# Kernel tuning notes

Hardware: AMD Instinct MI355X
Metric: run time of the kernel (lower is better)

## Reference

```python
import jax, jax.numpy as jnp
import numpy as np

B, L, D = 2, 2048, 2048
NH, NKV = 16, 8
HD = D // NH            # 128
GQ = NH // NKV          # queries per kv head
THETA = 10000.0
SCALE = HD ** -0.5


def rope_tables(seq_len, dim, theta):
    inv_freq = 1.0 / theta ** (jnp.arange(0, dim, 2, dtype=jnp.float32) / dim)
    t = jnp.arange(seq_len, dtype=jnp.float32)
    freqs = jnp.outer(t, inv_freq)              # [L, dim/2]
    emb = jnp.concatenate([freqs, freqs], -1)   # [L, dim]
    return jnp.cos(emb), jnp.sin(emb)


def rotate_half(x):
    x1, x2 = jnp.split(x, 2, axis=-1)
    return jnp.concatenate([-x2, x1], -1)


def setup_inputs() -> dict:
    key = jax.random.key(0)
    ks = jax.random.split(key, 5)
    s = 0.02
    return {
        "x": jax.random.normal(ks[0], (B, L, D), jnp.float32),
        "Wq": jax.random.normal(ks[1], (NH * HD, D), jnp.float32) * s,
        "Wk": jax.random.normal(ks[2], (NKV * HD, D), jnp.float32) * s,
        "Wv": jax.random.normal(ks[3], (NKV * HD, D), jnp.float32) * s,
        "Wo": jax.random.normal(ks[4], (D, D), jnp.float32) * s,
    }


def reference(x, Wq, Wk, Wv, Wo):
    b, l, d = x.shape
    q = (x @ Wq.T).reshape(b, l, NH, HD).transpose(0, 2, 1, 3)    # [B,NH,L,HD]
    k = (x @ Wk.T).reshape(b, l, NKV, HD).transpose(0, 2, 1, 3)   # [B,NKV,L,HD]
    v = (x @ Wv.T).reshape(b, l, NKV, HD).transpose(0, 2, 1, 3)

    cos, sin = rope_tables(l, HD, THETA)                           # [L,HD]
    q = q * cos + rotate_half(q) * sin
    k = k * cos + rotate_half(k) * sin

    # GQA without materializing expanded K/V: group queries per kv head
    qg = q.reshape(b, NKV, GQ, l, HD)
    scores = jnp.einsum('bgrld,bgmd->bgrlm', qg, k) * SCALE        # [B,NKV,GQ,L,L]
    causal = jnp.triu(jnp.ones((l, l), bool), k=1)
    scores = jnp.where(causal, -jnp.inf, scores)
    attn = jax.nn.softmax(scores.astype(jnp.float32), axis=-1).astype(q.dtype)
    out = jnp.einsum('bgrlm,bgmd->bgrld', attn, v)                 # [B,NKV,GQ,L,HD]
    out = out.reshape(b, NH, l, HD).transpose(0, 2, 1, 3).reshape(b, l, d)
    return out @ Wo.T
```

## Files before the change

kernel.cpp:

```cpp
#include <hip/hip_runtime.h>
#include <cmath>

using u16 = unsigned short;
typedef u16    u16x4  __attribute__((ext_vector_type(4)));
typedef u16    u16x8  __attribute__((ext_vector_type(8)));
typedef __bf16 bf16x8 __attribute__((ext_vector_type(8)));
typedef float  f32x4  __attribute__((ext_vector_type(4)));

constexpr int Bc  = 2;
constexpr int Lc  = 2048;
constexpr int Dc  = 2048;
constexpr int NHc = 16;
constexpr int NKVc= 8;
constexpr int HDc = 128;

__device__ __forceinline__ u16 f2b(float f) {
  union { float f; unsigned u; } v; v.f = f;
  unsigned r = v.u + 0x7FFFu + ((v.u >> 16) & 1u);
  return (u16)(r >> 16);
}
__device__ __forceinline__ u16 f2b_fast(float f) {
  union { float f; unsigned u; } v; v.f = f;
  return (u16)((v.u + 0x8000u) >> 16);
}
__device__ __forceinline__ float b2f(u16 s) {
  union { unsigned u; float f; } v; v.u = ((unsigned)s) << 16;
  return v.f;
}
__device__ __forceinline__ bf16x8 ld_frag(const u16* p) {
  u16x8 u = *(const u16x8*)p;
  return __builtin_bit_cast(bf16x8, u);
}
__device__ __forceinline__ void gld_lds16(u16* ldst, const u16* gsrc) {
  __builtin_amdgcn_global_load_lds(
      (const __attribute__((address_space(1))) void*)gsrc,
      (__attribute__((address_space(3))) void*)ldst, 16, 0, 0);
}

__global__ void cvt_f32_bf16(const float* __restrict__ src, u16* __restrict__ dst, int n) {
  int i = (blockIdx.x * blockDim.x + threadIdx.x) * 4;
  if (i >= n) return;
  float4 v = *(const float4*)&src[i];
  u16x4 o = { f2b(v.x), f2b(v.y), f2b(v.z), f2b(v.w) };
  *(u16x4*)&dst[i] = o;
}

__global__ void cvt_w3(const float* __restrict__ Wq, const float* __restrict__ Wk,
                       const float* __restrict__ Wv, u16* __restrict__ dst) {
  const int n1 = Dc * Dc;
  const int n2 = n1 + (NKVc*HDc) * Dc;
  const int n3 = n2 + (NKVc*HDc) * Dc;
  int i = (blockIdx.x * blockDim.x + threadIdx.x) * 4;
  if (i >= n3) return;
  const float* src; int off;
  if (i < n1)      { src = Wq; off = i; }
  else if (i < n2) { src = Wk; off = i - n1; }
  else             { src = Wv; off = i - n2; }
  float4 v = *(const float4*)&src[off];
  u16x4 o = { f2b(v.x), f2b(v.y), f2b(v.z), f2b(v.w) };
  *(u16x4*)&dst[i] = o;
}

__device__ __forceinline__ void stage_tile32(u16* lds, const u16* __restrict__ A,
    const u16* __restrict__ W, int slot, int kt, int m0, int n0, int wave, int lane)
{
  const int srow = lane >> 2;
  const int scg  = lane & 3;
  const int skey = (lane >> 3) & 3;
  const int sb   = slot * 16384;
#pragma unroll
  for (int i = 0; i < 2; ++i) {
    int c = wave + i * 8;
    int row = c * 16 + srow;
    gld_lds16(&lds[sb + c * 512],
              &A[(size_t)(m0 + row) * Dc + kt * 32 + (scg ^ skey) * 8]);
    gld_lds16(&lds[sb + 8192 + c * 512],
              &W[(size_t)(n0 + row) * Dc + kt * 32 + (scg ^ skey) * 8]);
  }
}

__device__ __forceinline__ void compute_tile32(const u16* lds, int slot,
    int wm, int wn, int quad, int l16, f32x4 acc[8][4])
{
  const u16* sA = lds + slot * 16384;
  const u16* sB = sA + 8192;
  const int pcg = (quad ^ ((l16 >> 1) & 3)) * 8;
  bf16x8 af[8], bfr[4];
#pragma unroll
  for (int mi = 0; mi < 8; ++mi)
    af[mi] = ld_frag(&sA[(wm * 128 + mi * 16 + l16) * 32 + pcg]);
#pragma unroll
  for (int ni = 0; ni < 4; ++ni)
    bfr[ni] = ld_frag(&sB[(wn * 64 + ni * 16 + l16) * 32 + pcg]);
  __builtin_amdgcn_s_setprio(1);
#pragma unroll
  for (int mi = 0; mi < 8; ++mi)
#pragma unroll
    for (int ni = 0; ni < 4; ++ni)
      acc[mi][ni] = __builtin_amdgcn_mfma_f32_16x16x32_bf16(af[mi], bfr[ni], acc[mi][ni], 0, 0, 0);
  __builtin_amdgcn_s_setprio(0);
}

__global__ __launch_bounds__(512, 2) void gemm256_qkv(
    const u16* __restrict__ A, const u16* __restrict__ W,
    u16* __restrict__ Qp, u16* __restrict__ Kp, u16* __restrict__ Vtp)
{
  __shared__ u16 lds[65536];
  const int tid  = threadIdx.x;
  const int wave = tid >> 6, lane = tid & 63;
  const int quad = lane >> 4, l16 = lane & 15;
  const int bid = blockIdx.x;
  const int swz = (bid & 7) * 32 + (bid >> 3);
  const int tx = swz & 15, ty = swz >> 4;
  const int m0 = ty * 256, n0 = tx * 256;
  const int wm = wave >> 2, wn = wave & 3;

  f32x4 acc[8][4];
#pragma unroll
  for (int i = 0; i < 8; ++i)
#pragma unroll
    for (int j = 0; j < 4; ++j) acc[i][j] = {0.f, 0.f, 0.f, 0.f};

  stage_tile32(lds, A, W, 0, 0, m0, n0, wave, lane);
  stage_tile32(lds, A, W, 1, 1, m0, n0, wave, lane);
  stage_tile32(lds, A, W, 2, 2, m0, n0, wave, lane);

  for (int kt = 0; kt < 61; ++kt) {
    __asm__ volatile("s_waitcnt vmcnt(8)\n\ts_barrier" ::: "memory");
    stage_tile32(lds, A, W, (kt + 3) & 3, kt + 3, m0, n0, wave, lane);
    compute_tile32(lds, kt & 3, wm, wn, quad, l16, acc);
  }
  __asm__ volatile("s_waitcnt vmcnt(8)\n\ts_barrier" ::: "memory");
  compute_tile32(lds, 1, wm, wn, quad, l16, acc);
  __asm__ volatile("s_waitcnt vmcnt(4)\n\ts_barrier" ::: "memory");
  compute_tile32(lds, 2, wm, wn, quad, l16, acc);
  __asm__ volatile("s_waitcnt vmcnt(0)\n\ts_barrier" ::: "memory");
  compute_tile32(lds, 3, wm, wn, quad, l16, acc);

  if (n0 < 3072) {
    u16* Cb; int ldc, nc0;
    if (n0 < 2048) { Cb = Qp; ldc = 2048; nc0 = n0; }
    else           { Cb = Kp; ldc = 1024; nc0 = n0 - 2048; }
#pragma unroll
    for (int mi = 0; mi < 8; ++mi)
#pragma unroll
      for (int ni = 0; ni < 4; ++ni)
#pragma unroll
        for (int r = 0; r < 4; ++r) {
          int m = m0 + wm * 128 + mi * 16 + quad * 4 + r;
          int n = nc0 + wn * 64 + ni * 16 + l16;
          Cb[(size_t)m * ldc + n] = f2b(acc[mi][ni][r]);
        }
  } else {
    __syncthreads();
#pragma unroll
    for (int mi = 0; mi < 8; ++mi)
#pragma unroll
      for (int ni = 0; ni < 4; ++ni)
#pragma unroll
        for (int r = 0; r < 4; ++r) {
          int l = wm * 128 + mi * 16 + quad * 4 + r;
          int d = wn * 64 + ni * 16 + l16;
          lds[l * 256 + (((d >> 3) ^ (l & 31)) << 3) + (d & 7)] = f2b(acc[mi][ni][r]);
        }
    __syncthreads();
    const int b    = m0 >> 11;
    const int hkv0 = (n0 - 3072) >> 7;
#pragma unroll
    for (int it = 0; it < 16; ++it) {
      int sl = tid + it * 512;
      int dl = sl >> 5;
      int lc = (sl & 31) * 8;
      u16x8 v;
#pragma unroll
      for (int e = 0; e < 8; ++e) {
        int l = lc + e;
        v[e] = lds[l * 256 + (((dl >> 3) ^ (l & 31)) << 3) + (dl & 7)];
      }
      const int hkv = hkv0 + (dl >> 7);
      const int d   = dl & 127;
      *(u16x8*)&Vtp[(((size_t)b * NKVc + hkv) * HDc + d) * (size_t)Lc + (m0 & (Lc - 1)) + lc] = v;
    }
  }
}

__global__ __launch_bounds__(256) void gemm_out(
    const u16* __restrict__ A, const u16* __restrict__ W,
    float* __restrict__ Cf, int M, int N, int K)
{
  __shared__ u16 lds[16384];
  u16* lA = lds;
  u16* lB = lds + 8192;
  const int tid  = threadIdx.x;
  const int wave = tid >> 6, lane = tid & 63;
  const int quad = lane >> 4, l16 = lane & 15;
  const int t7   = l16 & 7;
  const int m0 = blockIdx.y * 128, n0 = blockIdx.x * 128;
  const int mw = (wave >> 1) * 64, nw = (wave & 1) * 64;
  const int r8 = lane >> 3;
  const int cgl = (lane & 7) ^ r8;

  f32x4 acc[4][4];
#pragma unroll
  for (int i = 0; i < 4; ++i)
#pragma unroll
    for (int j = 0; j < 4; ++j) acc[i][j] = {0.f, 0.f, 0.f, 0.f};

  for (int kt = 0; kt < K; kt += 64) {
#pragma unroll
    for (int cc = 0; cc < 4; ++cc) {
      int c = wave + cc * 4;
      gld_lds16(&lA[c * 512], &A[(size_t)(m0 + 8 * c + r8) * K + kt + cgl * 8]);
      gld_lds16(&lB[c * 512], &W[(size_t)(n0 + 8 * c + r8) * K + kt + cgl * 8]);
    }
    __syncthreads();
#pragma unroll
    for (int s = 0; s < 2; ++s) {
      bf16x8 af[4], bf[4];
#pragma unroll
      for (int i = 0; i < 4; ++i)
        af[i] = ld_frag(&lA[(mw + i*16 + l16) * 64 + ((quad + 4*s) ^ t7) * 8]);
#pragma unroll
      for (int j = 0; j < 4; ++j)
        bf[j] = ld_frag(&lB[(nw + j*16 + l16) * 64 + ((quad + 4*s) ^ t7) * 8]);
#pragma unroll
      for (int i = 0; i < 4; ++i)
#pragma unroll
        for (int j = 0; j < 4; ++j)
          acc[i][j] = __builtin_amdgcn_mfma_f32_16x16x32_bf16(af[i], bf[j], acc[i][j], 0, 0, 0);
    }
    __syncthreads();
  }

#pragma unroll
  for (int i = 0; i < 4; ++i)
#pragma unroll
    for (int j = 0; j < 4; ++j)
#pragma unroll
      for (int r = 0; r < 4; ++r) {
        int m = m0 + mw + i*16 + quad*4 + r;
        int n = n0 + nw + j*16 + l16;
        Cf[(size_t)m * N + n] = acc[i][j][r];
      }
}

__global__ void rope2_kernel(u16* __restrict__ Qp, u16* __restrict__ Kp, float qs)
{
  const int nQ = Bc * Lc * NHc * 64;
  const int nT = nQ + Bc * Lc * NKVc * 64;
  int t = blockIdx.x * blockDim.x + threadIdx.x;
  if (t >= nT) return;
  u16* T; int nheads; float osc; int idx;
  if (t < nQ) { T = Qp; nheads = NHc;  osc = qs;  idx = t; }
  else        { T = Kp; nheads = NKVc; osc = 1.f; idx = t - nQ; }
  int d   = idx & 63;
  int h   = (idx >> 6) % nheads;
  int row = idx / (nheads * 64);
  int l   = row & (Lc - 1);
  float freq = exp2f((float)d * (-13.287712379549449f / 64.f));
  float ang  = (float)l * freq;
  float s, c;
  sincosf(ang, &s, &c);
  size_t base = (size_t)row * (nheads * 128) + h * 128;
  float x1 = b2f(T[base + d]);
  float x2 = b2f(T[base + d + 64]);
  T[base + d]      = f2b((x1 * c - x2 * s) * osc);
  T[base + d + 64] = f2b((x2 * c + x1 * s) * osc);
}

__global__ __launch_bounds__(512) void flash_kernel(
    const u16* __restrict__ Q, const u16* __restrict__ K, const u16* __restrict__ Vt,
    u16* __restrict__ O)
{
  __shared__ u16 smem[41984];
  const int tid  = threadIdx.x;
  const int wave = tid >> 6, lane = tid & 63;
  const int quad = lane >> 4, l16 = lane & 15;
  const int hw = wave >> 2, wr = wave & 3;
  const int bhkv = blockIdx.x;
  const int b = bhkv >> 3, hkv = bhkv & 7;
  const int h = hkv * 2 + hw;

  const size_t kbase = ((size_t)b * Lc) * (NKVc * HDc) + (size_t)hkv * HDc;
  const size_t vbase = (((size_t)b * NKVc + hkv) * HDc) * (size_t)Lc;

  const int kr8 = lane >> 4;
  const int kcl = lane & 15;
  const int vr16 = lane >> 3;
  const int vkl  = lane & 7;

  u16* sP_w = smem + 32768 + wave * 1152;

  for (int pass = 0; pass < 2; ++pass) {
    const int qt = (pass == 0) ? (31 - (int)blockIdx.y) : (int)blockIdx.y;
    const int q0 = qt * 64;

    __syncthreads();
#pragma unroll
    for (int i = 0; i < 4; ++i) {
      int g = tid + i * 512;
      int row = g >> 4, cg = g & 15;
      int qh = hkv * 2 + (row >> 6);
      int rr = row & 63;
      *(u16x8*)&smem[row * 128 + (cg ^ (row & 15)) * 8] =
          *(const u16x8*)&Q[((size_t)(b * Lc + q0 + rr)) * Dc + (size_t)qh * HDc + cg * 8];
    }
    __syncthreads();
    bf16x8 qf[4];
#pragma unroll
    for (int ks = 0; ks < 4; ++ks)
      qf[ks] = ld_frag(&smem[(hw*64 + wr*16 + l16) * 128 + ((ks*4 + quad) ^ l16) * 8]);
    __syncthreads();

#pragma unroll
    for (int i = 0; i < 2; ++i) {
      int c = wave + i * 8;
      int row = c * 4 + kr8;
      gld_lds16(smem + c * 512,
                &K[kbase + (size_t)row * (NKVc*HDc) + (size_t)(kcl ^ (row & 15)) * 8]);
    }
#pragma unroll
    for (int i = 0; i < 2; ++i) {
      int c = wave + i * 8;
      int d = c * 8 + vr16;
      gld_lds16(smem + 16384 + c * 512,
                &Vt[vbase + (size_t)d * Lc + (size_t)(vkl ^ (d & 7)) * 8]);
    }

    f32x4 acc_o[8];
#pragma unroll
    for (int i = 0; i < 8; ++i) acc_o[i] = {0.f, 0.f, 0.f, 0.f};
    float ps[4] = {0.f, 0.f, 0.f, 0.f};

    for (int kt = 0; kt <= qt; ++kt) {
      const int kOff  = (kt & 1) ? 8192 : 0;
      const int kOffN = (kt & 1) ? 0 : 8192;
      const int vOff  = (kt & 1) ? 24576 : 16384;
      const int vOffN = (kt & 1) ? 16384 : 24576;

      __asm__ volatile("s_waitcnt vmcnt(2)\n\ts_barrier" ::: "memory");

      if (kt < qt) {
#pragma unroll
        for (int i = 0; i < 2; ++i) {
          int c = wave + i * 8;
          int row = (kt + 1) * 64 + c * 4 + kr8;
          gld_lds16(smem + kOffN + c * 512,
                    &K[kbase + (size_t)row * (NKVc*HDc) + (size_t)(kcl ^ (row & 15)) * 8]);
        }
      }

      const u16* sKc = smem + kOff;
      f32x4 accs[4];
#pragma unroll
      for (int n = 0; n < 4; ++n) accs[n] = {0.f, 0.f, 0.f, 0.f};
#pragma unroll
      for (int ks = 0; ks < 4; ++ks)
#pragma unroll
        for (int n = 0; n < 4; ++n) {
          bf16x8 kf = ld_frag(&sKc[(n*16 + l16) * 128 + ((ks*4 + quad) ^ l16) * 8]);
          accs[n] = __builtin_amdgcn_mfma_f32_16x16x32_bf16(qf[ks], kf, accs[n], 0, 0, 0);
        }

      const int qrow = q0 + wr*16 + quad*4;
      if (kt == qt) {
#pragma unroll
        for (int n = 0; n < 4; ++n) {
          int kg = kt*64 + n*16 + l16;
#pragma unroll
          for (int r = 0; r < 4; ++r)
            if (kg > qrow + r) accs[n][r] = -INFINITY;
        }
      }
#pragma unroll
      for (int n = 0; n < 4; ++n)
#pragma unroll
        for (int r = 0; r < 4; ++r) {
          float p = exp2f(accs[n][r]);
          accs[n][r] = p;
          ps[r] += p;
        }

#pragma unroll
      for (int n = 0; n < 4; ++n)
#pragma unroll
        for (int r = 0; r < 4; ++r)
          sP_w[(quad*4 + r) * 72 + n*16 + l16] = f2b_fast(accs[n][r]);

      if (kt < qt)
        __asm__ volatile("s_waitcnt vmcnt(2) lgkmcnt(0)\n\ts_barrier" ::: "memory");
      else
        __asm__ volatile("s_waitcnt vmcnt(0) lgkmcnt(0)\n\ts_barrier" ::: "memory");

      if (kt < qt) {
#pragma unroll
        for (int i = 0; i < 2; ++i) {
          int c = wave + i * 8;
          int d = c * 8 + vr16;
          gld_lds16(smem + vOffN + c * 512,
                    &Vt[vbase + (size_t)d * Lc + (kt+1)*64 + (size_t)(vkl ^ (d & 7)) * 8]);
        }
      }

      const u16* sVc = smem + vOff;
#pragma unroll
      for (int s2 = 0; s2 < 2; ++s2) {
        bf16x8 pf = ld_frag(&sP_w[l16 * 72 + s2*32 + quad*8]);
#pragma unroll
        for (int di = 0; di < 8; ++di) {
          bf16x8 vf = ld_frag(&sVc[(di*16 + l16) * 64 + ((s2*4 + quad) ^ (l16 & 7)) * 8]);
          acc_o[di] = __builtin_amdgcn_mfma_f32_16x16x32_bf16(pf, vf, acc_o[di], 0, 0, 0);
        }
      }
    }

#pragma unroll
    for (int off = 1; off < 16; off <<= 1)
#pragma unroll
      for (int r = 0; r < 4; ++r) ps[r] += __shfl_xor(ps[r], off);
    float inv[4];
#pragma unroll
    for (int r = 0; r < 4; ++r) inv[r] = 1.0f / ps[r];

#pragma unroll
    for (int di = 0; di < 8; ++di)
#pragma unroll
      for (int r = 0; r < 4; ++r) {
        int qrow = q0 + wr*16 + quad*4 + r;
        int d = di*16 + l16;
        float v = acc_o[di][r] * inv[r];
        O[((size_t)(b * Lc + qrow)) * Dc + (size_t)h * HDc + d] = f2b(v);
      }
  }
}

extern "C" void kernel_launch(void* const* d_in, const int* in_sizes, int n_in,
                              void* d_out, int out_size, void* d_ws, size_t ws_size,
                              hipStream_t stream)
{
  const float* x  = (const float*)d_in[0];
  const float* Wq = (const float*)d_in[1];
  const float* Wk = (const float*)d_in[2];
  const float* Wv = (const float*)d_in[3];
  const float* Wo = (const float*)d_in[4];
  float* out = (float*)d_out;

  const int M = Bc * Lc;
  u16* ws = (u16*)d_ws;
  u16* xb   = ws;
  u16* Ow   = xb;
  u16* Wcat = ws + (size_t)8 * 1024 * 1024;
  u16* Wob  = Wcat;
  u16* Qw   = Wcat + (size_t)8 * 1024 * 1024;
  u16* Kw   = Qw   + (size_t)8 * 1024 * 1024;
  u16* Vt   = Kw   + (size_t)4 * 1024 * 1024;

  const int nx = M * Dc;
  const int nq = Dc * Dc;
  const int nw3 = nq + 2 * (NKVc*HDc) * Dc;
  cvt_f32_bf16<<<nx/1024, 256, 0, stream>>>(x, xb, nx);
  cvt_w3<<<nw3/1024, 256, 0, stream>>>(Wq, Wk, Wv, Wcat);

  gemm256_qkv<<<256, 512, 0, stream>>>(xb, Wcat, Qw, Kw, Vt);

  const float qs = 0.08838834764831845f * 1.4426950408889634f;
  const int nrope = M * (NHc + NKVc) * 64;
  rope2_kernel<<<(nrope + 255) / 256, 256, 0, stream>>>(Qw, Kw, qs);

  flash_kernel<<<dim3(Bc*NKVc, 16), 512, 0, stream>>>(Qw, Kw, Vt, Ow);

  cvt_f32_bf16<<<nq/1024, 256, 0, stream>>>(Wo, Wob, nq);
  gemm_out<<<dim3(16, 32), 256, 0, stream>>>(Ow, Wob, out, M, Dc, Dc);
}
```

Baseline: 337.8 us.

## Restructure QKV GEMM main loop into ping-pong K=64 tiles with interleaved staging

Replaces the 4-slot K=32 ring buffer in the fused QKV projection GEMM with two K=64 A/B buffers and a hand-scheduled loop. Each iteration splits compute into quarter-tile MFMA groups, interleaving fragment reads, global-to-LDS staging and barriers with setprio hints, in the style of HipKittens' 8-wave ping-pong. The aim is to overlap memory traffic with MFMA issue and cut per-K-step barrier overhead. The cost is many more barriers and fragile manual waitcnt accounting, which could stall or race if the counts are wrong.

```diff
diff --git a/kernel.cpp b/kernel.cpp
--- a/kernel.cpp
+++ b/kernel.cpp
@@ -61,45 +61,34 @@
   *(u16x4*)&dst[i] = o;
 }
 
-__device__ __forceinline__ void stage_tile32(u16* lds, const u16* __restrict__ A,
-    const u16* __restrict__ W, int slot, int kt, int m0, int n0, int wave, int lane)
-{
-  const int srow = lane >> 2;
-  const int scg  = lane & 3;
-  const int skey = (lane >> 3) & 3;
-  const int sb   = slot * 16384;
-#pragma unroll
-  for (int i = 0; i < 2; ++i) {
-    int c = wave + i * 8;
-    int row = c * 16 + srow;
-    gld_lds16(&lds[sb + c * 512],
-              &A[(size_t)(m0 + row) * Dc + kt * 32 + (scg ^ skey) * 8]);
-    gld_lds16(&lds[sb + 8192 + c * 512],
-              &W[(size_t)(n0 + row) * Dc + kt * 32 + (scg ^ skey) * 8]);
-  }
-}
-
-__device__ __forceinline__ void compute_tile32(const u16* lds, int slot,
-    int wm, int wn, int quad, int l16, f32x4 acc[8][4])
-{
-  const u16* sA = lds + slot * 16384;
-  const u16* sB = sA + 8192;
-  const int pcg = (quad ^ ((l16 >> 1) & 3)) * 8;
-  bf16x8 af[8], bfr[4];
-#pragma unroll
-  for (int mi = 0; mi < 8; ++mi)
-    af[mi] = ld_frag(&sA[(wm * 128 + mi * 16 + l16) * 32 + pcg]);
-#pragma unroll
-  for (int ni = 0; ni < 4; ++ni)
-    bfr[ni] = ld_frag(&sB[(wn * 64 + ni * 16 + l16) * 32 + pcg]);
-  __builtin_amdgcn_s_setprio(1);
-#pragma unroll
-  for (int mi = 0; mi < 8; ++mi)
-#pragma unroll
-    for (int ni = 0; ni < 4; ++ni)
-      acc[mi][ni] = __builtin_amdgcn_mfma_f32_16x16x32_bf16(af[mi], bfr[ni], acc[mi][ni], 0, 0, 0);
-  __builtin_amdgcn_s_setprio(0);
-}
+#define MFMA_(a, b, c) __builtin_amdgcn_mfma_f32_16x16x32_bf16(a, b, c, 0, 0, 0)
+#define BAR()   __builtin_amdgcn_s_barrier()
+#define LGKM0() { __asm__ volatile("s_waitcnt lgkmcnt(0)" ::: "memory"); \
+                  __builtin_amdgcn_sched_barrier(0); }
+#define PRIO1() __builtin_amdgcn_s_setprio(1)
+#define PRIO0() __builtin_amdgcn_s_setprio(0)
+
+#define STG(lb, gp, goff, h, kc)                                          \
+  { _Pragma("unroll")                                                     \
+    for (int i_ = 0; i_ < 2; ++i_) {                                      \
+      int c_ = wave + (i_ << 3);                                          \
+      gld_lds16((lb) + (h) * 8192 + c_ * 512,                             \
+                (gp) + (goff) + (size_t)(h) * 262144 + (size_t)c_ * 16384 + (kc)); } }
+
+#define LDA_(bA, mi, kk) ld_frag((bA) + ((wm << 7) + ((mi) << 4) + l16) * 64 + \
+                                 (((quad + ((kk) << 2)) ^ t7) << 3))
+#define LDB_(bB, ni, kk) ld_frag((bB) + ((wn << 6) + ((ni) << 4) + l16) * 64 + \
+                                 (((quad + ((kk) << 2)) ^ t7) << 3))
+
+#define QUAD_MFMA(MI0, NI0, BARR)                                                      \
+  { _Pragma("unroll")                                                                  \
+    for (int mi_ = 0; mi_ < 4; ++mi_) {                                                \
+      _Pragma("unroll")                                                                \
+      for (int ni_ = 0; ni_ < 2; ++ni_) {                                              \
+        acc[(MI0)+mi_][(NI0)+ni_] =                                                    \
+            MFMA_(aF[mi_][0], BARR[ni_][0], acc[(MI0)+mi_][(NI0)+ni_]);                \
+        acc[(MI0)+mi_][(NI0)+ni_] =                                                    \
+            MFMA_(aF[mi_][1], BARR[ni_][1], acc[(MI0)+mi_][(NI0)+ni_]); } } }
 
 __global__ __launch_bounds__(512, 2) void gemm256_qkv(
     const u16* __restrict__ A, const u16* __restrict__ W,
@@ -108,34 +97,95 @@
   __shared__ u16 lds[65536];
   const int tid  = threadIdx.x;
   const int wave = tid >> 6, lane = tid & 63;
-  const int quad = lane >> 4, l16 = lane & 15;
+  const int quad = lane >> 4, l16 = lane & 15, t7 = l16 & 7;
   const int bid = blockIdx.x;
   const int swz = (bid & 7) * 32 + (bid >> 3);
   const int tx = swz & 15, ty = swz >> 4;
   const int m0 = ty * 256, n0 = tx * 256;
   const int wm = wave >> 2, wn = wave & 3;
+  const int srow = lane >> 3;
+  const int sx8  = ((lane & 7) ^ srow) << 3;
+
+  u16* const A0L = lds;
+  u16* const B0L = lds + 16384;
+  u16* const A1L = lds + 32768;
+  u16* const B1L = lds + 49152;
+
+  const size_t aOff = (size_t)(m0 + srow) * 2048 + sx8;
+  const size_t bOff = (size_t)(n0 + srow) * 2048 + sx8;
 
   f32x4 acc[8][4];
 #pragma unroll
   for (int i = 0; i < 8; ++i)
 #pragma unroll
     for (int j = 0; j < 4; ++j) acc[i][j] = {0.f, 0.f, 0.f, 0.f};
-
-  stage_tile32(lds, A, W, 0, 0, m0, n0, wave, lane);
-  stage_tile32(lds, A, W, 1, 1, m0, n0, wave, lane);
-  stage_tile32(lds, A, W, 2, 2, m0, n0, wave, lane);
-
-  for (int kt = 0; kt < 61; ++kt) {
-    __asm__ volatile("s_waitcnt vmcnt(8)\n\ts_barrier" ::: "memory");
-    stage_tile32(lds, A, W, (kt + 3) & 3, kt + 3, m0, n0, wave, lane);
-    compute_tile32(lds, kt & 3, wm, wn, quad, l16, acc);
+  bf16x8 aF[4][2], bL[2][2], bH[2][2];
+
+  STG(A0L, A, aOff, 0, 0);  STG(A0L, A, aOff, 1, 0);
+  STG(B0L, W, bOff, 0, 0);  STG(B0L, W, bOff, 1, 0);
+  STG(B1L, W, bOff, 0, 64); STG(B1L, W, bOff, 1, 64);
+  __asm__ volatile("s_waitcnt vmcnt(4)" ::: "memory");
+  BAR();
+
+  int kc = 0;
+  for (int it = 0; it < 16; ++it, kc += 128) {
+    const bool st2 = (it < 15);
+#pragma unroll
+    for (int mi = 0; mi < 4; ++mi) { aF[mi][0] = LDA_(A0L, mi, 0); aF[mi][1] = LDA_(A0L, mi, 1); }
+#pragma unroll
+    for (int ni = 0; ni < 2; ++ni) { bL[ni][0] = LDB_(B0L, ni, 0); bL[ni][1] = LDB_(B0L, ni, 1); }
+    STG(A1L, A, aOff, 0, kc + 64);
+    __asm__ volatile("s_waitcnt lgkmcnt(8)" ::: "memory");
+    BAR(); LGKM0(); PRIO1();
+    QUAD_MFMA(0, 0, bL);
+    PRIO0(); BAR();
+#pragma unroll
+    for (int ni = 0; ni < 2; ++ni) { bH[ni][0] = LDB_(B0L, 2 + ni, 0); bH[ni][1] = LDB_(B0L, 2 + ni, 1); }
+    STG(A1L, A, aOff, 1, kc + 64);
+    BAR(); LGKM0(); PRIO1();
+    QUAD_MFMA(0, 2, bH);
+    PRIO0(); BAR();
+#pragma unroll
+    for (int mi = 0; mi < 4; ++mi) { aF[mi][0] = LDA_(A0L, 4 + mi, 0); aF[mi][1] = LDA_(A0L, 4 + mi, 1); }
+    if (st2) STG(B0L, W, bOff, 0, kc + 128);
+    BAR(); LGKM0(); PRIO1();
+    QUAD_MFMA(4, 0, bL);
+    PRIO0(); BAR();
+    if (st2) STG(B0L, W, bOff, 1, kc + 128);
+    BAR(); PRIO1();
+    QUAD_MFMA(4, 2, bH);
+    PRIO0();
+    if (st2) { __asm__ volatile("s_waitcnt vmcnt(4)" ::: "memory"); }
+    else     { __asm__ volatile("s_waitcnt vmcnt(0)" ::: "memory"); }
+    BAR();
+#pragma unroll
+    for (int mi = 0; mi < 4; ++mi) { aF[mi][0] = LDA_(A1L, mi, 0); aF[mi][1] = LDA_(A1L, mi, 1); }
+#pragma unroll
+    for (int ni = 0; ni < 2; ++ni) { bL[ni][0] = LDB_(B1L, ni, 0); bL[ni][1] = LDB_(B1L, ni, 1); }
+    if (st2) STG(A0L, A, aOff, 0, kc + 128);
+    __asm__ volatile("s_waitcnt lgkmcnt(8)" ::: "memory");
+    BAR(); LGKM0(); PRIO1();
+    QUAD_MFMA(0, 0, bL);
+    PRIO0(); BAR();
+#pragma unroll
+    for (int ni = 0; ni < 2; ++ni) { bH[ni][0] = LDB_(B1L, 2 + ni, 0); bH[ni][1] = LDB_(B1L, 2 + ni, 1); }
+    if (st2) STG(A0L, A, aOff, 1, kc + 128);
+    BAR(); LGKM0(); PRIO1();
+    QUAD_MFMA(0, 2, bH);
+    PRIO0(); BAR();
+#pragma unroll
+    for (int mi = 0; mi < 4; ++mi) { aF[mi][0] = LDA_(A1L, 4 + mi, 0); aF[mi][1] = LDA_(A1L, 4 + mi, 1); }
+    if (st2) STG(B1L, W, bOff, 0, kc + 192);
+    BAR(); LGKM0(); PRIO1();
+    QUAD_MFMA(4, 0, bL);
+    PRIO0(); BAR();
+    if (st2) STG(B1L, W, bOff, 1, kc + 192);
+    BAR(); PRIO1();
+    QUAD_MFMA(4, 2, bH);
+    PRIO0();
+    if (st2) { __asm__ volatile("s_waitcnt vmcnt(4)" ::: "memory"); }
+    BAR();
   }
-  __asm__ volatile("s_waitcnt vmcnt(8)\n\ts_barrier" ::: "memory");
-  compute_tile32(lds, 1, wm, wn, quad, l16, acc);
-  __asm__ volatile("s_waitcnt vmcnt(4)\n\ts_barrier" ::: "memory");
-  compute_tile32(lds, 2, wm, wn, quad, l16, acc);
-  __asm__ volatile("s_waitcnt vmcnt(0)\n\ts_barrier" ::: "memory");
-  compute_tile32(lds, 3, wm, wn, quad, l16, acc);
 
   if (n0 < 3072) {
     u16* Cb; int ldc, nc0;
@@ -167,8 +217,8 @@
     const int b    = m0 >> 11;
     const int hkv0 = (n0 - 3072) >> 7;
 #pragma unroll
-    for (int it = 0; it < 16; ++it) {
-      int sl = tid + it * 512;
+    for (int it2 = 0; it2 < 16; ++it2) {
+      int sl = tid + it2 * 512;
       int dl = sl >> 5;
       int lc = (sl & 31) * 8;
       u16x8 v;
@@ -183,6 +233,10 @@
     }
   }
 }
+#undef STG
+#undef LDA_
+#undef LDB_
+#undef QUAD_MFMA
 
 __global__ __launch_bounds__(256) void gemm_out(
     const u16* __restrict__ A, const u16* __restrict__ W,
```

New measurement: 339.4 us. Within noise of the previous version (+0.5%).
